# Kernel optimization log

Hardware: AMD Instinct MI355X
Metric: run time of the kernel (lower is better)

Reference implementation:

```python
import jax, jax.numpy as jnp
import numpy as np

N_NODES = 100000
N_EDGES = 3200000
IN_FEAT = 512
HIDDEN = 256
N_CLASS = 40


def setup_inputs() -> dict:
    key = jax.random.key(0)
    ks = jax.random.split(key, 6)
    x = jax.random.normal(ks[0], (N_NODES, IN_FEAT), dtype=jnp.float32)
    w1 = jax.random.uniform(ks[1], (IN_FEAT, HIDDEN), dtype=jnp.float32)
    b1 = jnp.zeros((HIDDEN,), dtype=jnp.float32)
    w2 = jax.random.uniform(ks[2], (HIDDEN, N_CLASS), dtype=jnp.float32)
    b2 = jnp.zeros((N_CLASS,), dtype=jnp.float32)
    edge_val = jax.random.uniform(ks[3], (N_EDGES,), dtype=jnp.float32)
    edge_row = jax.random.randint(ks[4], (N_EDGES,), 0, N_NODES, dtype=jnp.int32)
    edge_col = jax.random.randint(ks[5], (N_EDGES,), 0, N_NODES, dtype=jnp.int32)
    return {"x": x, "w1": w1, "b1": b1, "w2": w2, "b2": b2,
            "edge_val": edge_val, "edge_row": edge_row, "edge_col": edge_col}


def _graph_conv(h, w, b, edge_val, edge_row, edge_col, n_nodes):
    # dense transform: [N, d_in] @ [d_in, d_out]
    support = h @ w
    # sparse adj @ support via gather + segment_sum (COO SpMM)
    msgs = edge_val[:, None] * support[edge_col]          # [E, d_out]
    agg = jax.ops.segment_sum(msgs, edge_row, num_segments=n_nodes)
    return agg + b


def reference(x, w1, b1, w2, b2, edge_val, edge_row, edge_col):
    n = x.shape[0]
    h = jax.nn.relu(_graph_conv(x, w1, b1, edge_val, edge_row, edge_col, n))
    # dropout is identity in eval mode (training=False)
    out = _graph_conv(h, w2, b2, edge_val, edge_row, edge_col, n)
    return jax.nn.log_softmax(out, axis=1)
```

## Files before the change

### kernel.cpp

```cpp
#include <hip/hip_runtime.h>
#include <cstdint>
#include <cstddef>

#define N_NODES 100000
#define N_EDGES 3200000
#define IN_FEAT 512
#define HIDDEN  256
#define N_CLASS 40
#define S2_STRIDE 48

#define N_BUCKETS 196
#define SC_CHUNK 4096
#define N_SC_BLOCKS 782

#define OFF_SUPPORT1 ((size_t)0)
#define OFF_H        ((size_t)51200000)
#define OFF_SUPPORT2 ((size_t)102400000)
#define OFF_W1T      ((size_t)121600000)
#define OFF_RPTR     ((size_t)121862144)
#define OFF_BCNT     ((size_t)122262272)
#define OFF_BBASE    ((size_t)122263296)
#define OFF_BCUR     ((size_t)122264320)
#define OFF_BINNED   ((size_t)122265344)
#define OFF_SEDGE    ((size_t)147865344)

typedef __attribute__((ext_vector_type(8))) short short8x;
typedef __attribute__((ext_vector_type(4))) float f32x4;
typedef __attribute__((ext_vector_type(8))) unsigned short u16x8;

static __device__ __forceinline__ unsigned short f2bf(float f) {
  unsigned u = __float_as_uint(f);
  unsigned r = (u + 0x7FFFu + ((u >> 16) & 1u)) >> 16;
  return (unsigned short)r;
}
static __device__ __forceinline__ float bf2f(unsigned short s) {
  return __uint_as_float(((unsigned)s) << 16);
}

__global__ __launch_bounds__(256) void k_bincnt(const int* __restrict__ erow,
                                                int* __restrict__ bcnt) {
  __shared__ int lh[256];
  lh[threadIdx.x] = 0;
  __syncthreads();
  int i = blockIdx.x * blockDim.x + threadIdx.x;
  int stride = gridDim.x * blockDim.x;
  for (; i < N_EDGES; i += stride) atomicAdd(&lh[erow[i] >> 9], 1);
  __syncthreads();
  if (threadIdx.x < N_BUCKETS) atomicAdd(&bcnt[threadIdx.x], lh[threadIdx.x]);
}

__global__ __launch_bounds__(256) void k_binscan(const int* __restrict__ bcnt,
                                                 int* __restrict__ bbase,
                                                 int* __restrict__ bcur,
                                                 int* __restrict__ rptr) {
  __shared__ int s[256];
  int t = threadIdx.x;
  int v = (t < N_BUCKETS) ? bcnt[t] : 0;
  s[t] = v;
  __syncthreads();
  for (int off = 1; off < 256; off <<= 1) {
    int y = (t >= off) ? s[t - off] : 0;
    __syncthreads();
    s[t] += y;
    __syncthreads();
  }
  if (t < N_BUCKETS) {
    int e = s[t] - v;
    bbase[t] = e;
    bcur[t] = e;
  }
  if (t == 0) {
    bbase[N_BUCKETS] = N_EDGES;
    rptr[N_NODES] = N_EDGES;
  }
}

__global__ __launch_bounds__(256) void k_binscatter(const int* __restrict__ erow,
                                                    const int* __restrict__ ecol,
                                                    const float* __restrict__ eval,
                                                    int* __restrict__ bcur,
                                                    int2* __restrict__ binned) {
  __shared__ int lcnt[256];
  __shared__ int lcur[256];
  const int t = threadIdx.x;
  const int base = blockIdx.x * SC_CHUNK;
  lcnt[t] = 0;
  __syncthreads();
  int rows[16], cols[16], vals[16];
#pragma unroll
  for (int e = 0; e < 16; e++) {
    int i = base + t + e * 256;
    if (i < N_EDGES) {
      rows[e] = erow[i];
      cols[e] = ecol[i];
      vals[e] = __float_as_int(eval[i]);
      atomicAdd(&lcnt[rows[e] >> 9], 1);
    } else {
      rows[e] = -1;
    }
  }
  __syncthreads();
  if (t < N_BUCKETS) lcur[t] = atomicAdd(&bcur[t], lcnt[t]);
  __syncthreads();
#pragma unroll
  for (int e = 0; e < 16; e++) {
    if (rows[e] >= 0) {
      int bkt = rows[e] >> 9;
      int p = atomicAdd(&lcur[bkt], 1);
      binned[p] = make_int2(((rows[e] & 511) << 17) | cols[e], vals[e]);
    }
  }
}

__global__ __launch_bounds__(256) void k_bucket_csr(const int2* __restrict__ binned,
                                                    const int* __restrict__ bbase,
                                                    int* __restrict__ rptr,
                                                    int2* __restrict__ sedge) {
  const int b = blockIdx.x;
  const int t = threadIdx.x;
  __shared__ int cnt[512];
  __shared__ int excl[512];
  __shared__ int s[256];
  cnt[t] = 0;
  cnt[t + 256] = 0;
  __syncthreads();
  const int ebase = bbase[b];
  const int ecnt = bbase[b + 1] - ebase;
  for (int i = t; i < ecnt; i += 256)
    atomicAdd(&cnt[((unsigned)binned[ebase + i].x) >> 17], 1);
  __syncthreads();
  int c0 = cnt[2 * t], c1 = cnt[2 * t + 1];
  s[t] = c0 + c1;
  __syncthreads();
  for (int off = 1; off < 256; off <<= 1) {
    int y = (t >= off) ? s[t - off] : 0;
    __syncthreads();
    s[t] += y;
    __syncthreads();
  }
  int e = s[t] - (c0 + c1);
  excl[2 * t] = e;
  excl[2 * t + 1] = e + c0;
  __syncthreads();
  for (int i = t; i < 512; i += 256) {
    int node = b * 512 + i;
    if (node < N_NODES) rptr[node] = ebase + excl[i];
  }
  __syncthreads();
  for (int i = t; i < ecnt; i += 256) {
    int2 e2 = binned[ebase + i];
    int lrow = ((unsigned)e2.x) >> 17;
    int col = e2.x & 0x1FFFF;
    int p = atomicAdd(&excl[lrow], 1);
    sedge[ebase + p] = make_int2(col, e2.y);
  }
}

__global__ __launch_bounds__(256) void k_prep_w(const float* __restrict__ W,
                                                unsigned short* __restrict__ Wt) {
  int tid = blockIdx.x * 256 + threadIdx.x;
  int n = tid & 255;
  int k = tid >> 8;
  Wt[(size_t)n * IN_FEAT + k] = f2bf(W[(size_t)k * HIDDEN + n]);
}

__global__ __launch_bounds__(256) void k_gemm1(const float* __restrict__ X,
                                               const unsigned short* __restrict__ Wt,
                                               unsigned short* __restrict__ C) {
  __shared__ short As[128 * 32];
  __shared__ short Bs[256 * 32];
  const int t = threadIdx.x;
  const int wave = t >> 6, lane = t & 63;
  const int q = lane >> 4, r = lane & 15;
  const int wm = (wave >> 1) * 64;
  const int wn = (wave & 1) * 128;
  const int m0 = blockIdx.x * 128;

  f32x4 acc[4][8];
#pragma unroll
  for (int mi = 0; mi < 4; mi++)
#pragma unroll
    for (int ni = 0; ni < 8; ni++) acc[mi][ni] = (f32x4){0.f, 0.f, 0.f, 0.f};

  for (int k0 = 0; k0 < IN_FEAT; k0 += 32) {
#pragma unroll
    for (int i = 0; i < 2; i++) {
      int cidx = t + i * 256;
      int row = cidx >> 2;
      int ko = (cidx & 3) * 8;
      int gr = m0 + row;
      if (gr > N_NODES - 1) gr = N_NODES - 1;
      const float4* src = (const float4*)&X[(size_t)gr * IN_FEAT + k0 + ko];
      float4 x0 = src[0], x1 = src[1];
      short8x a;
      a[0] = (short)f2bf(x0.x); a[1] = (short)f2bf(x0.y);
      a[2] = (short)f2bf(x0.z); a[3] = (short)f2bf(x0.w);
      a[4] = (short)f2bf(x1.x); a[5] = (short)f2bf(x1.y);
      a[6] = (short)f2bf(x1.z); a[7] = (short)f2bf(x1.w);
      *(short8x*)&As[row * 32 + ko] = a;
    }
#pragma unroll
    for (int i = 0; i < 4; i++) {
      int cidx = t + i * 256;
      int row = cidx >> 2;
      int ko = (cidx & 3) * 8;
      short8x b = *(const short8x*)&Wt[(size_t)row * IN_FEAT + k0 + ko];
      *(short8x*)&Bs[row * 32 + ko] = b;
    }
    __syncthreads();
    short8x af[4], bf[8];
#pragma unroll
    for (int mi = 0; mi < 4; mi++)
      af[mi] = *(const short8x*)&As[(wm + mi * 16 + r) * 32 + q * 8];
#pragma unroll
    for (int ni = 0; ni < 8; ni++)
      bf[ni] = *(const short8x*)&Bs[(wn + ni * 16 + r) * 32 + q * 8];
#pragma unroll
    for (int mi = 0; mi < 4; mi++)
#pragma unroll
      for (int ni = 0; ni < 8; ni++)
        acc[mi][ni] = __builtin_amdgcn_mfma_f32_16x16x32_bf16(af[mi], bf[ni],
                                                              acc[mi][ni], 0, 0, 0);
    __syncthreads();
  }
#pragma unroll
  for (int mi = 0; mi < 4; mi++) {
#pragma unroll
    for (int ni = 0; ni < 8; ni++) {
      int col = wn + ni * 16 + r;
#pragma unroll
      for (int reg = 0; reg < 4; reg++) {
        int row = m0 + wm + mi * 16 + q * 4 + reg;
        if (row < N_NODES)
          C[(size_t)row * HIDDEN + col] = f2bf(acc[mi][ni][reg]);
      }
    }
  }
}

__global__ __launch_bounds__(256) void k_spmm1(const unsigned short* __restrict__ S,
                                               const int* __restrict__ rptr,
                                               const int2* __restrict__ sedge,
                                               const float* __restrict__ b1,
                                               unsigned short* __restrict__ H) {
  const int node = (blockIdx.x * blockDim.x + threadIdx.x) >> 6;
  const int lane = threadIdx.x & 63;
  const int half = lane >> 5;
  const int fl = lane & 31;
  int e0 = rptr[node], e1 = rptr[node + 1];
  float a[8];
#pragma unroll
  for (int k = 0; k < 8; k++) a[k] = 0.f;
  for (int base = e0; base < e1; base += 64) {
    int rem = min(64, e1 - base);
    int c = 0;
    float v = 0.f;
    if (lane < rem) {
      int2 e = sedge[base + lane];
      c = e.x;
      v = __int_as_float(e.y);
    }
    int iters = (rem + 1) >> 1;
#pragma unroll 4
    for (int j = 0; j < iters; j++) {
      int idx = 2 * j + half;
      int cj = __shfl(c, idx);
      float vj = __shfl(v, idx);
      short8x s8 = *(const short8x*)&S[(size_t)cj * HIDDEN + fl * 8];
#pragma unroll
      for (int k = 0; k < 8; k++)
        a[k] += vj * bf2f((unsigned short)s8[k]);
    }
  }
#pragma unroll
  for (int k = 0; k < 8; k++) a[k] += __shfl_xor(a[k], 32);
  if (half == 0) {
    float4 b0 = *(const float4*)&b1[fl * 8];
    float4 b4 = *(const float4*)&b1[fl * 8 + 4];
    u16x8 o;
    o[0] = f2bf(fmaxf(a[0] + b0.x, 0.f));
    o[1] = f2bf(fmaxf(a[1] + b0.y, 0.f));
    o[2] = f2bf(fmaxf(a[2] + b0.z, 0.f));
    o[3] = f2bf(fmaxf(a[3] + b0.w, 0.f));
    o[4] = f2bf(fmaxf(a[4] + b4.x, 0.f));
    o[5] = f2bf(fmaxf(a[5] + b4.y, 0.f));
    o[6] = f2bf(fmaxf(a[6] + b4.z, 0.f));
    o[7] = f2bf(fmaxf(a[7] + b4.w, 0.f));
    *(u16x8*)&H[(size_t)node * HIDDEN + fl * 8] = o;
  }
}

__global__ __launch_bounds__(256) void k_gemm2(const unsigned short* __restrict__ H,
                                               const float* __restrict__ W2,
                                               float* __restrict__ S2) {
  __shared__ __align__(16) float Ws[HIDDEN][N_CLASS];
  __shared__ float Hs[256][33];
  const int t = threadIdx.x;
  const int r0 = blockIdx.x * 256;

#pragma unroll
  for (int i = 0; i < 10; i++) {
    int qq = t + i * 256;
    float4 w = *(const float4*)&W2[(size_t)qq * 4];
    *(float4*)&((float*)Ws)[(size_t)qq * 4] = w;
  }

  float acc[N_CLASS];
#pragma unroll
  for (int n = 0; n < N_CLASS; n++) acc[n] = 0.f;

  for (int kc = 0; kc < HIDDEN; kc += 32) {
    __syncthreads();
#pragma unroll
    for (int i = 0; i < 8; i++) {
      int qq = t + i * 256;
      int row = qq >> 3;
      int kv = (qq & 7) * 4;
      int grow = r0 + row;
      if (grow > N_NODES - 1) grow = N_NODES - 1;
      ushort4 hv = *(const ushort4*)&H[(size_t)grow * HIDDEN + kc + kv];
      Hs[row][kv + 0] = bf2f(hv.x);
      Hs[row][kv + 1] = bf2f(hv.y);
      Hs[row][kv + 2] = bf2f(hv.z);
      Hs[row][kv + 3] = bf2f(hv.w);
    }
    __syncthreads();
    const float4* Wsv = (const float4*)Ws;
#pragma unroll
    for (int k = 0; k < 32; k++) {
      float hk = Hs[t][k];
      int kg = kc + k;
#pragma unroll
      for (int n4 = 0; n4 < 10; n4++) {
        float4 w = Wsv[kg * 10 + n4];
        acc[n4 * 4 + 0] += hk * w.x;
        acc[n4 * 4 + 1] += hk * w.y;
        acc[n4 * 4 + 2] += hk * w.z;
        acc[n4 * 4 + 3] += hk * w.w;
      }
    }
  }
  int row = r0 + t;
  if (row < N_NODES) {
#pragma unroll
    for (int n4 = 0; n4 < 10; n4++) {
      float4 o = {acc[n4 * 4 + 0], acc[n4 * 4 + 1], acc[n4 * 4 + 2], acc[n4 * 4 + 3]};
      *(float4*)&S2[(size_t)row * S2_STRIDE + n4 * 4] = o;
    }
    float4 z = {0.f, 0.f, 0.f, 0.f};
    *(float4*)&S2[(size_t)row * S2_STRIDE + 40] = z;
    *(float4*)&S2[(size_t)row * S2_STRIDE + 44] = z;
  }
}

__global__ __launch_bounds__(256) void k_spmm2(const float* __restrict__ S2,
                                               const int* __restrict__ rptr,
                                               const int2* __restrict__ sedge,
                                               const float* __restrict__ b2,
                                               float* __restrict__ out) {
  const int node = (blockIdx.x * blockDim.x + threadIdx.x) >> 6;
  const int lane = threadIdx.x & 63;
  const int q = lane >> 4;
  const int fl = lane & 15;
  int e0 = rptr[node], e1 = rptr[node + 1];
  float a[3] = {0.f, 0.f, 0.f};
  for (int base = e0; base < e1; base += 64) {
    int rem = min(64, e1 - base);
    int c = 0;
    float v = 0.f;
    if (lane < rem) {
      int2 e = sedge[base + lane];
      c = e.x;
      v = __int_as_float(e.y);
    }
    int iters = (rem + 3) >> 2;
#pragma unroll 2
    for (int j = 0; j < iters; j++) {
      int idx = 4 * j + q;
      int cj = __shfl(c, idx);
      float vj = __shfl(v, idx);
      const float* row = &S2[(size_t)cj * S2_STRIDE + fl * 3];
      a[0] += vj * row[0];
      a[1] += vj * row[1];
      a[2] += vj * row[2];
    }
  }
#pragma unroll
  for (int k = 0; k < 3; k++) {
    a[k] += __shfl_xor(a[k], 16);
    a[k] += __shfl_xor(a[k], 32);
  }
  float x[3];
  float mloc = -INFINITY;
#pragma unroll
  for (int k = 0; k < 3; k++) {
    int f = fl * 3 + k;
    x[k] = (f < N_CLASS) ? (a[k] + b2[f]) : -INFINITY;
    mloc = fmaxf(mloc, x[k]);
  }
#pragma unroll
  for (int o = 1; o < 16; o <<= 1) mloc = fmaxf(mloc, __shfl_xor(mloc, o));
  float sloc = 0.f;
#pragma unroll
  for (int k = 0; k < 3; k++)
    sloc += (fl * 3 + k < N_CLASS) ? expf(x[k] - mloc) : 0.f;
#pragma unroll
  for (int o = 1; o < 16; o <<= 1) sloc += __shfl_xor(sloc, o);
  float ls = logf(sloc);
  if (q == 0) {
#pragma unroll
    for (int k = 0; k < 3; k++) {
      int f = fl * 3 + k;
      if (f < N_CLASS) out[(size_t)node * N_CLASS + f] = (x[k] - mloc) - ls;
    }
  }
}

extern "C" void kernel_launch(void* const* d_in, const int* in_sizes, int n_in,
                              void* d_out, int out_size, void* d_ws, size_t ws_size,
                              hipStream_t stream) {
  const float* x    = (const float*)d_in[0];
  const float* w1   = (const float*)d_in[1];
  const float* b1   = (const float*)d_in[2];
  const float* w2   = (const float*)d_in[3];
  const float* b2   = (const float*)d_in[4];
  const float* eval = (const float*)d_in[5];
  const int*   erow = (const int*)d_in[6];
  const int*   ecol = (const int*)d_in[7];
  float* out = (float*)d_out;

  char* ws = (char*)d_ws;
  unsigned short* support1 = (unsigned short*)(ws + OFF_SUPPORT1);
  unsigned short* h        = (unsigned short*)(ws + OFF_H);
  float* support2 = (float*)(ws + OFF_SUPPORT2);
  unsigned short* w1t = (unsigned short*)(ws + OFF_W1T);
  int*   rptr   = (int*)(ws + OFF_RPTR);
  int*   bcnt   = (int*)(ws + OFF_BCNT);
  int*   bbase  = (int*)(ws + OFF_BBASE);
  int*   bcur   = (int*)(ws + OFF_BCUR);
  int2*  binned = (int2*)(ws + OFF_BINNED);
  int2*  sedge  = (int2*)(ws + OFF_SEDGE);

  hipMemsetAsync(bcnt, 0, N_BUCKETS * 4, stream);
  k_prep_w<<<512, 256, 0, stream>>>(w1, w1t);
  k_bincnt<<<512, 256, 0, stream>>>(erow, bcnt);
  k_binscan<<<1, 256, 0, stream>>>(bcnt, bbase, bcur, rptr);
  k_binscatter<<<N_SC_BLOCKS, 256, 0, stream>>>(erow, ecol, eval, bcur, binned);
  k_bucket_csr<<<N_BUCKETS, 256, 0, stream>>>(binned, bbase, rptr, sedge);

  k_gemm1<<<dim3((N_NODES + 127) / 128, 1), 256, 0, stream>>>(x, w1t, support1);
  k_spmm1<<<N_NODES / 4, 256, 0, stream>>>(support1, rptr, sedge, b1, h);

  k_gemm2<<<(N_NODES + 255) / 256, 256, 0, stream>>>(h, w2, support2);
  k_spmm2<<<N_NODES / 4, 256, 0, stream>>>(support2, rptr, sedge, b2, out);
}
```

Before: 863.6 us.

## Store layer-2 support in bf16 and fuse weight prep into bin count

Layer-2 support rows are now stored as packed bf16 instead of fp32, which halves the bytes gathered per edge in the second SpMM. The SpMM2 lane mapping changes so each lane reads 6 features via a 12-byte load and 8 edges are processed in parallel per wave. The W1 transpose/convert kernel is merged into the bin-count kernel to save a launch, and the SpMM1 unroll factor goes from 4 to 8. The cost is extra rounding error in the layer-2 aggregation.

```diff
diff --git a/kernel.cpp b/kernel.cpp
--- a/kernel.cpp
+++ b/kernel.cpp
@@ -16,17 +16,19 @@
 #define OFF_SUPPORT1 ((size_t)0)
 #define OFF_H        ((size_t)51200000)
 #define OFF_SUPPORT2 ((size_t)102400000)
-#define OFF_W1T      ((size_t)121600000)
-#define OFF_RPTR     ((size_t)121862144)
-#define OFF_BCNT     ((size_t)122262272)
-#define OFF_BBASE    ((size_t)122263296)
-#define OFF_BCUR     ((size_t)122264320)
-#define OFF_BINNED   ((size_t)122265344)
-#define OFF_SEDGE    ((size_t)147865344)
+#define OFF_W1T      ((size_t)112000000)
+#define OFF_RPTR     ((size_t)112262144)
+#define OFF_BCNT     ((size_t)112662272)
+#define OFF_BBASE    ((size_t)112663296)
+#define OFF_BCUR     ((size_t)112664320)
+#define OFF_BINNED   ((size_t)112665344)
+#define OFF_SEDGE    ((size_t)138265344)
 
 typedef __attribute__((ext_vector_type(8))) short short8x;
 typedef __attribute__((ext_vector_type(4))) float f32x4;
 typedef __attribute__((ext_vector_type(8))) unsigned short u16x8;
+typedef __attribute__((ext_vector_type(3))) unsigned int u32x3;
+typedef __attribute__((ext_vector_type(4))) unsigned int u32x4;
 
 static __device__ __forceinline__ unsigned short f2bf(float f) {
   unsigned u = __float_as_uint(f);
@@ -36,13 +38,27 @@
 static __device__ __forceinline__ float bf2f(unsigned short s) {
   return __uint_as_float(((unsigned)s) << 16);
 }
+static __device__ __forceinline__ float bflo(unsigned u) {
+  return __uint_as_float(u << 16);
+}
+static __device__ __forceinline__ float bfhi(unsigned u) {
+  return __uint_as_float(u & 0xFFFF0000u);
+}
 
 __global__ __launch_bounds__(256) void k_bincnt(const int* __restrict__ erow,
-                                                int* __restrict__ bcnt) {
+                                                int* __restrict__ bcnt,
+                                                const float* __restrict__ W,
+                                                unsigned short* __restrict__ Wt) {
+  int tid = blockIdx.x * 256 + threadIdx.x;
+  {
+    int n = tid & 255;
+    int k = tid >> 8;
+    Wt[(size_t)n * IN_FEAT + k] = f2bf(W[(size_t)k * HIDDEN + n]);
+  }
   __shared__ int lh[256];
   lh[threadIdx.x] = 0;
   __syncthreads();
-  int i = blockIdx.x * blockDim.x + threadIdx.x;
+  int i = tid;
   int stride = gridDim.x * blockDim.x;
   for (; i < N_EDGES; i += stride) atomicAdd(&lh[erow[i] >> 9], 1);
   __syncthreads();
@@ -154,14 +170,6 @@
     int p = atomicAdd(&excl[lrow], 1);
     sedge[ebase + p] = make_int2(col, e2.y);
   }
-}
-
-__global__ __launch_bounds__(256) void k_prep_w(const float* __restrict__ W,
-                                                unsigned short* __restrict__ Wt) {
-  int tid = blockIdx.x * 256 + threadIdx.x;
-  int n = tid & 255;
-  int k = tid >> 8;
-  Wt[(size_t)n * IN_FEAT + k] = f2bf(W[(size_t)k * HIDDEN + n]);
 }
 
 __global__ __launch_bounds__(256) void k_gemm1(const float* __restrict__ X,
@@ -261,7 +269,7 @@
       v = __int_as_float(e.y);
     }
     int iters = (rem + 1) >> 1;
-#pragma unroll 4
+#pragma unroll 8
     for (int j = 0; j < iters; j++) {
       int idx = 2 * j + half;
       int cj = __shfl(c, idx);
@@ -292,7 +300,7 @@
 
 __global__ __launch_bounds__(256) void k_gemm2(const unsigned short* __restrict__ H,
                                                const float* __restrict__ W2,
-                                               float* __restrict__ S2) {
+                                               unsigned short* __restrict__ S2) {
   __shared__ __align__(16) float Ws[HIDDEN][N_CLASS];
   __shared__ float Hs[256][33];
   const int t = threadIdx.x;
@@ -342,28 +350,32 @@
   }
   int row = r0 + t;
   if (row < N_NODES) {
-#pragma unroll
-    for (int n4 = 0; n4 < 10; n4++) {
-      float4 o = {acc[n4 * 4 + 0], acc[n4 * 4 + 1], acc[n4 * 4 + 2], acc[n4 * 4 + 3]};
-      *(float4*)&S2[(size_t)row * S2_STRIDE + n4 * 4] = o;
-    }
-    float4 z = {0.f, 0.f, 0.f, 0.f};
-    *(float4*)&S2[(size_t)row * S2_STRIDE + 40] = z;
-    *(float4*)&S2[(size_t)row * S2_STRIDE + 44] = z;
-  }
-}
-
-__global__ __launch_bounds__(256) void k_spmm2(const float* __restrict__ S2,
+    unsigned pk[24];
+#pragma unroll
+    for (int i = 0; i < 20; i++)
+      pk[i] = (unsigned)f2bf(acc[2 * i]) | ((unsigned)f2bf(acc[2 * i + 1]) << 16);
+#pragma unroll
+    for (int i = 20; i < 24; i++) pk[i] = 0;
+    unsigned* dst = (unsigned*)&S2[(size_t)row * S2_STRIDE];
+#pragma unroll
+    for (int i = 0; i < 6; i++) {
+      u32x4 o = {pk[4 * i], pk[4 * i + 1], pk[4 * i + 2], pk[4 * i + 3]};
+      *(u32x4*)&dst[4 * i] = o;
+    }
+  }
+}
+
+__global__ __launch_bounds__(256) void k_spmm2(const unsigned short* __restrict__ S2,
                                                const int* __restrict__ rptr,
                                                const int2* __restrict__ sedge,
                                                const float* __restrict__ b2,
                                                float* __restrict__ out) {
   const int node = (blockIdx.x * blockDim.x + threadIdx.x) >> 6;
   const int lane = threadIdx.x & 63;
-  const int q = lane >> 4;
-  const int fl = lane & 15;
+  const int q = lane >> 3;
+  const int fl = lane & 7;
   int e0 = rptr[node], e1 = rptr[node + 1];
-  float a[3] = {0.f, 0.f, 0.f};
+  float a[6] = {0.f, 0.f, 0.f, 0.f, 0.f, 0.f};
   for (int base = e0; base < e1; base += 64) {
     int rem = min(64, e1 - base);
     int c = 0;
@@ -373,44 +385,48 @@
       c = e.x;
       v = __int_as_float(e.y);
     }
-    int iters = (rem + 3) >> 2;
-#pragma unroll 2
+    int iters = (rem + 7) >> 3;
+#pragma unroll 4
     for (int j = 0; j < iters; j++) {
-      int idx = 4 * j + q;
+      int idx = 8 * j + q;
       int cj = __shfl(c, idx);
       float vj = __shfl(v, idx);
-      const float* row = &S2[(size_t)cj * S2_STRIDE + fl * 3];
-      a[0] += vj * row[0];
-      a[1] += vj * row[1];
-      a[2] += vj * row[2];
-    }
-  }
-#pragma unroll
-  for (int k = 0; k < 3; k++) {
+      u32x3 w = *(const u32x3*)&S2[(size_t)cj * S2_STRIDE + fl * 6];
+      a[0] += vj * bflo(w.x);
+      a[1] += vj * bfhi(w.x);
+      a[2] += vj * bflo(w.y);
+      a[3] += vj * bfhi(w.y);
+      a[4] += vj * bflo(w.z);
+      a[5] += vj * bfhi(w.z);
+    }
+  }
+#pragma unroll
+  for (int k = 0; k < 6; k++) {
+    a[k] += __shfl_xor(a[k], 8);
     a[k] += __shfl_xor(a[k], 16);
     a[k] += __shfl_xor(a[k], 32);
   }
-  float x[3];
+  float x[6];
   float mloc = -INFINITY;
 #pragma unroll
-  for (int k = 0; k < 3; k++) {
-    int f = fl * 3 + k;
+  for (int k = 0; k < 6; k++) {
+    int f = fl * 6 + k;
     x[k] = (f < N_CLASS) ? (a[k] + b2[f]) : -INFINITY;
     mloc = fmaxf(mloc, x[k]);
   }
 #pragma unroll
-  for (int o = 1; o < 16; o <<= 1) mloc = fmaxf(mloc, __shfl_xor(mloc, o));
+  for (int o = 1; o < 8; o <<= 1) mloc = fmaxf(mloc, __shfl_xor(mloc, o));
   float sloc = 0.f;
 #pragma unroll
-  for (int k = 0; k < 3; k++)
-    sloc += (fl * 3 + k < N_CLASS) ? expf(x[k] - mloc) : 0.f;
-#pragma unroll
-  for (int o = 1; o < 16; o <<= 1) sloc += __shfl_xor(sloc, o);
+  for (int k = 0; k < 6; k++)
+    sloc += (fl * 6 + k < N_CLASS) ? expf(x[k] - mloc) : 0.f;
+#pragma unroll
+  for (int o = 1; o < 8; o <<= 1) sloc += __shfl_xor(sloc, o);
   float ls = logf(sloc);
   if (q == 0) {
 #pragma unroll
-    for (int k = 0; k < 3; k++) {
-      int f = fl * 3 + k;
+    for (int k = 0; k < 6; k++) {
+      int f = fl * 6 + k;
       if (f < N_CLASS) out[(size_t)node * N_CLASS + f] = (x[k] - mloc) - ls;
     }
   }
@@ -432,7 +448,7 @@
   char* ws = (char*)d_ws;
   unsigned short* support1 = (unsigned short*)(ws + OFF_SUPPORT1);
   unsigned short* h        = (unsigned short*)(ws + OFF_H);
-  float* support2 = (float*)(ws + OFF_SUPPORT2);
+  unsigned short* support2 = (unsigned short*)(ws + OFF_SUPPORT2);
   unsigned short* w1t = (unsigned short*)(ws + OFF_W1T);
   int*   rptr   = (int*)(ws + OFF_RPTR);
   int*   bcnt   = (int*)(ws + OFF_BCNT);
@@ -442,8 +458,7 @@
   int2*  sedge  = (int2*)(ws + OFF_SEDGE);
 
   hipMemsetAsync(bcnt, 0, N_BUCKETS * 4, stream);
-  k_prep_w<<<512, 256, 0, stream>>>(w1, w1t);
-  k_bincnt<<<512, 256, 0, stream>>>(erow, bcnt);
+  k_bincnt<<<512, 256, 0, stream>>>(erow, bcnt, w1, w1t);
   k_binscan<<<1, 256, 0, stream>>>(bcnt, bbase, bcur, rptr);
   k_binscatter<<<N_SC_BLOCKS, 256, 0, stream>>>(erow, ecol, eval, bcur, binned);
   k_bucket_csr<<<N_BUCKETS, 256, 0, stream>>>(binned, bbase, rptr, sedge);
```

Result: no change. 860.8 us (-0.3%).
